# Performance work log

Measured on AMD Instinct MI355X. Metric: run time of the kernel, lower is better.

The kernel has to match this reference:

```python
import jax, jax.numpy as jnp
import numpy as np

B, N, D, H = 1, 4096, 768, 12
HD = D // H
SCALE = HD ** -0.5

def setup_inputs() -> dict:
    key = jax.random.key(0)
    k1, k2, k3 = jax.random.split(key, 3)
    x = jax.random.normal(k1, (B, N, D), dtype=jnp.float32)
    W_qkv = jax.random.normal(k2, (D, 3 * D), dtype=jnp.float32) * (D ** -0.5)
    W_out = jax.random.normal(k3, (D, D), dtype=jnp.float32) * (D ** -0.5)
    b_out = jnp.zeros((D,), dtype=jnp.float32)
    return {"x": x, "W_qkv": W_qkv, "W_out": W_out, "b_out": b_out}

def reference(x, W_qkv, W_out, b_out):
    # qkv projection: (B,N,3D)
    qkv = x @ W_qkv
    q, k, v = jnp.split(qkv, 3, axis=-1)
    # (B,N,D) -> (B,H,N,hd)
    def heads(t):
        return t.reshape(B, N, H, HD).transpose(0, 2, 1, 3)
    q, k, v = heads(q), heads(k), heads(v)
    scores = jnp.einsum('bhnd,bhmd->bhnm', q, k) * SCALE  # (B,H,N,N)
    attn = jax.nn.softmax(scores, axis=-1)
    out = jnp.einsum('bhnm,bhmd->bhnd', attn, v)
    out = out.transpose(0, 2, 1, 3).reshape(B, N, D)
    return out @ W_out + b_out
```

## Files before the change

### kernel.cpp

```cpp
#include <hip/hip_runtime.h>
#include <hip/hip_bf16.h>
#include <math.h>

typedef __attribute__((ext_vector_type(8))) short bf16x8;
typedef __attribute__((ext_vector_type(4))) short bf16x4;
typedef __attribute__((ext_vector_type(4))) float floatx4;

constexpr int kN  = 4096;
constexpr int kD  = 768;
constexpr int kH  = 12;
constexpr int kHD = 64;
constexpr int k3D = 2304;
constexpr float kQScale = 0.18033688011112042f;

static __device__ __forceinline__ short f2b(float f) {
    __hip_bfloat16 h = __float2bfloat16(f);
    return *reinterpret_cast<short*>(&h);
}

static __device__ __forceinline__ float fast_exp2(float x) {
#if __has_builtin(__builtin_amdgcn_exp2f)
    return __builtin_amdgcn_exp2f(x);
#else
    return exp2f(x);
#endif
}

static __device__ __forceinline__ void async_copy16(const void* g, void* l) {
    __builtin_amdgcn_global_load_lds(
        (const __attribute__((address_space(1))) void*)g,
        (__attribute__((address_space(3))) void*)l, 16, 0, 0);
}

constexpr int kBlkX  = 1536;
constexpr int kBlkWq = 72 * 24;
constexpr int kBlkWo = 24 * 24;

__global__ __launch_bounds__(256)
void prep(const float* __restrict__ x, const float* __restrict__ Wq,
          const float* __restrict__ Wo, short* __restrict__ Xb,
          short* __restrict__ WqT, short* __restrict__ WoT)
{
    const int bid = blockIdx.x;
    const int tid = threadIdx.x;
    if (bid < kBlkX) {
        const int i = bid * 256 + tid;
        const float4* s = reinterpret_cast<const float4*>(x + (size_t)i * 8);
        float4 a = s[0], b = s[1];
        bf16x8 v;
        v[0] = f2b(a.x); v[1] = f2b(a.y); v[2] = f2b(a.z); v[3] = f2b(a.w);
        v[4] = f2b(b.x); v[5] = f2b(b.y); v[6] = f2b(b.z); v[7] = f2b(b.w);
        *reinterpret_cast<bf16x8*>(Xb + (size_t)i * 8) = v;
        return;
    }
    const float* src; short* dst; int R, C, bx, by;
    if (bid < kBlkX + kBlkWq) {
        const int local = bid - kBlkX;
        src = Wq; dst = WqT; R = kD; C = k3D; bx = local % 72; by = local / 72;
    } else {
        const int local = bid - kBlkX - kBlkWq;
        src = Wo; dst = WoT; R = kD; C = kD; bx = local % 24; by = local / 24;
    }
    __shared__ float t[32][33];
    const int c0 = bx * 32, r0 = by * 32;
    const int tx = tid & 31, ty = tid >> 5;
    #pragma unroll
    for (int i = ty; i < 32; i += 8)
        t[i][tx] = src[(size_t)(r0 + i) * C + c0 + tx];
    __syncthreads();
    #pragma unroll
    for (int i = ty; i < 32; i += 8)
        dst[(size_t)(c0 + i) * R + r0 + tx] = f2b(t[tx][i]);
}

template<int MODE>
__device__ __forceinline__
void gemm_core(const short* __restrict__ A, const short* __restrict__ BT,
               const float* __restrict__ bias, float* __restrict__ Cout,
               short* __restrict__ Qh, short* __restrict__ Kh, short* __restrict__ Vt,
               int N, int K)
{
    const int bm   = blockIdx.x * 128;
    const int bn   = blockIdx.y * 128;
    const int tid  = threadIdx.x;
    const int wave = tid >> 6;
    const int lane = tid & 63;
    const int l15  = lane & 15;
    const int quad = lane >> 4;
    const int l3   = l15 & 3;

    __shared__ alignas(16) short As[128 * 32];
    __shared__ alignas(16) short Bs[128 * 32];

    floatx4 acc[4][4] = {};
    const int wm = (wave >> 1) * 64;
    const int wn = (wave & 1) * 64;

    const int srl = lane >> 2;
    const int scc = (lane & 3) ^ (srl & 3);

    for (int k0 = 0; k0 < K; k0 += 32) {
        __syncthreads();
        #pragma unroll
        for (int j = 0; j < 2; ++j) {
            const int rs = 32 * wave + 16 * j;
            async_copy16(&A [(size_t)(bm + rs + srl) * K + k0 + 8 * scc], &As[rs * 32]);
            async_copy16(&BT[(size_t)(bn + rs + srl) * K + k0 + 8 * scc], &Bs[rs * 32]);
        }
        __syncthreads();

        bf16x8 af[4], bfr[4];
        #pragma unroll
        for (int mt = 0; mt < 4; ++mt)
            af[mt] = *reinterpret_cast<const bf16x8*>(&As[(wm + 16 * mt + l15) * 32 + 8 * (quad ^ l3)]);
        #pragma unroll
        for (int nt = 0; nt < 4; ++nt)
            bfr[nt] = *reinterpret_cast<const bf16x8*>(&Bs[(wn + 16 * nt + l15) * 32 + 8 * (quad ^ l3)]);
        #pragma unroll
        for (int mt = 0; mt < 4; ++mt)
            #pragma unroll
            for (int nt = 0; nt < 4; ++nt)
                acc[mt][nt] = __builtin_amdgcn_mfma_f32_16x16x32_bf16(af[mt], bfr[nt], acc[mt][nt], 0, 0, 0);
    }

    #pragma unroll
    for (int mt = 0; mt < 4; ++mt) {
        #pragma unroll
        for (int nt = 0; nt < 4; ++nt) {
            #pragma unroll
            for (int r = 0; r < 4; ++r) {
                const int row = bm + wm + mt * 16 + 4 * quad + r;
                const int col = bn + wn + nt * 16 + l15;
                float v = acc[mt][nt][r];
                if (MODE == 0) {
                    Cout[(size_t)row * N + col] = v + bias[col];
                } else {
                    const int proj   = col / kD;
                    const int within = col - proj * kD;
                    const int h = within >> 6;
                    const int d = within & 63;
                    if (proj == 0)      Qh[((size_t)h * kN + row) * kHD + d] = f2b(v * kQScale);
                    else if (proj == 1) Kh[((size_t)h * kN + row) * kHD + d] = f2b(v);
                    else                Vt[((size_t)h * kHD + d) * kN + row] = f2b(v);
                }
            }
        }
    }
}

__global__ __launch_bounds__(256)
void gemm_qkv(const short* __restrict__ A, const short* __restrict__ BT,
              short* __restrict__ Qh, short* __restrict__ Kh, short* __restrict__ Vt)
{
    gemm_core<1>(A, BT, nullptr, nullptr, Qh, Kh, Vt, k3D, kD);
}

__global__ __launch_bounds__(256)
void gemm_out(const short* __restrict__ A, const short* __restrict__ BT,
              const float* __restrict__ bias, float* __restrict__ Cout)
{
    gemm_core<0>(A, BT, bias, Cout, nullptr, nullptr, nullptr, kD, kD);
}

__global__ __launch_bounds__(256, 3)
void attn(const short* __restrict__ Qh, const short* __restrict__ Kh,
          const short* __restrict__ Vt, short* __restrict__ AO)
{
    const int h    = blockIdx.y;
    const int q0   = blockIdx.x * 64;
    const int tid  = threadIdx.x;
    const int wave = tid >> 6;
    const int lane = tid & 63;
    const int l15  = lane & 15;
    const int quad = lane >> 4;
    const int lx   = l15 & 7;
    const int px   = l15 & 3;

    __shared__ alignas(16) char smem[49920];
    short* Ks = (short*)smem;
    short* Vs = (short*)(smem + 16384);
    short* Pm = (short*)(smem + 32768);
    float* Red  = (float*)smem;
    float* Dred = (float*)(smem + 49152);

    short* Pw = Pm + wave * 2048;

    bf16x8 qf[4][2];
    #pragma unroll
    for (int mt = 0; mt < 4; ++mt) {
        const size_t qb = ((size_t)h * kN + q0 + 16 * mt + l15) * kHD + quad * 8;
        qf[mt][0] = *reinterpret_cast<const bf16x8*>(&Qh[qb]);
        qf[mt][1] = *reinterpret_cast<const bf16x8*>(&Qh[qb + 32]);
    }

    floatx4 oacc[4][4] = {};
    float psum[4] = {0.f, 0.f, 0.f, 0.f};

    const int krl = lane >> 3;
    const int kcc = (lane & 7) ^ (krl & 7);
    const int vrl = lane >> 4;
    const int vp  = lane & 15;

    for (int kv0 = 0; kv0 < kN; kv0 += 128) {
        __syncthreads();
        #pragma unroll
        for (int j = 0; j < 4; ++j) {
            const int rk = 32 * wave + 8 * j;
            async_copy16(&Kh[((size_t)h * kN + kv0 + rk + krl) * kHD + 8 * kcc],
                         &Ks[rk * 64]);
            const int rv0 = 16 * wave + 4 * j;
            const int rv  = rv0 + vrl;
            async_copy16(&Vt[((size_t)h * kHD + rv) * kN + kv0 + 8 * (vp ^ (rv & 7))],
                         &Vs[rv0 * 128]);
        }
        __syncthreads();

        #pragma unroll
        for (int nt = 0; nt < 2; ++nt) {
            const int krow = (32 * wave + 16 * nt + l15) * 64;
            bf16x8 kf0 = *reinterpret_cast<const bf16x8*>(&Ks[krow + 8 * (quad ^ lx)]);
            bf16x8 kf1 = *reinterpret_cast<const bf16x8*>(&Ks[krow + 8 * ((4 + quad) ^ lx)]);
            #pragma unroll
            for (int mt = 0; mt < 4; ++mt) {
                floatx4 sa = {};
                sa = __builtin_amdgcn_mfma_f32_16x16x32_bf16(kf0, qf[mt][0], sa, 0, 0, 0);
                sa = __builtin_amdgcn_mfma_f32_16x16x32_bf16(kf1, qf[mt][1], sa, 0, 0, 0);
                const float p0 = fast_exp2(sa[0]);
                const float p1 = fast_exp2(sa[1]);
                const float p2 = fast_exp2(sa[2]);
                const float p3 = fast_exp2(sa[3]);
                psum[mt] += (p0 + p1) + (p2 + p3);
                bf16x4 pk;
                pk[0] = f2b(p0); pk[1] = f2b(p1); pk[2] = f2b(p2); pk[3] = f2b(p3);
                *reinterpret_cast<bf16x4*>(
                    &Pw[(16 * mt + l15) * 32 + 8 * ((2 * nt + (quad >> 1)) ^ px) + 4 * (quad & 1)]) = pk;
            }
        }

        bf16x8 pa[4];
        #pragma unroll
        for (int mt = 0; mt < 4; ++mt)
            pa[mt] = *reinterpret_cast<const bf16x8*>(
                &Pw[(16 * mt + l15) * 32 + 8 * (quad ^ px)]);
        #pragma unroll
        for (int dt = 0; dt < 4; ++dt) {
            bf16x8 vv = *reinterpret_cast<const bf16x8*>(
                &Vs[(16 * dt + l15) * 128 + 8 * ((4 * wave + quad) ^ lx)]);
            #pragma unroll
            for (int mt = 0; mt < 4; ++mt)
                oacc[mt][dt] = __builtin_amdgcn_mfma_f32_16x16x32_bf16(pa[mt], vv, oacc[mt][dt], 0, 0, 0);
        }
    }

    #pragma unroll
    for (int mt = 0; mt < 4; ++mt) {
        psum[mt] += __shfl_xor(psum[mt], 16);
        psum[mt] += __shfl_xor(psum[mt], 32);
    }

    __syncthreads();
    if (wave > 0) {
        float* rb = Red + (wave - 1) * 4096;
        #pragma unroll
        for (int mt = 0; mt < 4; ++mt)
            #pragma unroll
            for (int dt = 0; dt < 4; ++dt)
                *reinterpret_cast<floatx4*>(&rb[((mt * 4 + dt) * 64 + lane) * 4]) = oacc[mt][dt];
        if (lane < 16) {
            #pragma unroll
            for (int mt = 0; mt < 4; ++mt)
                Dred[((wave - 1) * 4 + mt) * 16 + l15] = psum[mt];
        }
    }
    __syncthreads();
    if (wave == 0) {
        #pragma unroll
        for (int w = 0; w < 3; ++w) {
            const float* rb = Red + w * 4096;
            #pragma unroll
            for (int mt = 0; mt < 4; ++mt) {
                #pragma unroll
                for (int dt = 0; dt < 4; ++dt) {
                    floatx4 t = *reinterpret_cast<const floatx4*>(&rb[((mt * 4 + dt) * 64 + lane) * 4]);
                    oacc[mt][dt][0] += t[0];
                    oacc[mt][dt][1] += t[1];
                    oacc[mt][dt][2] += t[2];
                    oacc[mt][dt][3] += t[3];
                }
                psum[mt] += Dred[(w * 4 + mt) * 16 + l15];
            }
        }
        #pragma unroll
        for (int mt = 0; mt < 4; ++mt) {
            float lr[4];
            #pragma unroll
            for (int r = 0; r < 4; ++r)
                lr[r] = __shfl(psum[mt], 4 * quad + r);
            #pragma unroll
            for (int dt = 0; dt < 4; ++dt)
                #pragma unroll
                for (int r = 0; r < 4; ++r)
                    AO[(size_t)(q0 + 16 * mt + 4 * quad + r) * kD + h * kHD + 16 * dt + l15] =
                        f2b(oacc[mt][dt][r] / lr[r]);
        }
    }
}

extern "C" void kernel_launch(void* const* d_in, const int* in_sizes, int n_in,
                              void* d_out, int out_size, void* d_ws, size_t ws_size,
                              hipStream_t stream)
{
    const float* x     = (const float*)d_in[0];
    const float* W_qkv = (const float*)d_in[1];
    const float* W_out = (const float*)d_in[2];
    const float* b_out = (const float*)d_in[3];
    float* out = (float*)d_out;

    const size_t HNHD = (size_t)kH * kN * kHD;
    short* Qh    = (short*)d_ws;
    short* Kh    = Qh + HNHD;
    short* Vt    = Kh + HNHD;
    short* Xb    = Vt + HNHD;
    short* WqkvT = Xb + (size_t)kN * kD;
    short* WoutT = WqkvT + (size_t)k3D * kD;
    short* AO    = Xb;
    (void)in_sizes; (void)n_in; (void)out_size; (void)ws_size;

    prep<<<dim3(kBlkX + kBlkWq + kBlkWo), dim3(256), 0, stream>>>(
        x, W_qkv, W_out, Xb, WqkvT, WoutT);

    gemm_qkv<<<dim3(kN / 128, k3D / 128), dim3(256), 0, stream>>>(
        Xb, WqkvT, Qh, Kh, Vt);
    attn<<<dim3(kN / 64, kH), dim3(256), 0, stream>>>(Qh, Kh, Vt, AO);
    gemm_out<<<dim3(kN / 128, kD / 128), dim3(256), 0, stream>>>(
        AO, WoutT, b_out, out);
}
```

Measured before the change: 202.8 us.

## Load K/V fragments directly from global into registers with K prefetch, drop LDS staging

Attention kernel no longer stages K and V tiles through shared memory with async copies and block barriers. Each wave now reads its K and V MFMA fragments straight from global memory into registers and prefetches the next K tile one iteration ahead. The per-iteration __syncthreads pair is removed. Occupancy hint drops from 3 to 2 blocks per SM to leave room for the extra registers. The cost is scattered, less-coalesced global loads (especially strided V rows), relying on L2/L1 for reuse across the waves.

```diff
diff --git a/kernel.cpp b/kernel.cpp
--- a/kernel.cpp
+++ b/kernel.cpp
@@ -162,7 +162,7 @@
     gemm_core<0>(A, BT, bias, Cout, nullptr, nullptr, nullptr, kD, kD);
 }
 
-__global__ __launch_bounds__(256, 3)
+__global__ __launch_bounds__(256, 2)
 void attn(const short* __restrict__ Qh, const short* __restrict__ Kh,
           const short* __restrict__ Vt, short* __restrict__ AO)
 {
@@ -173,13 +173,10 @@
     const int lane = tid & 63;
     const int l15  = lane & 15;
     const int quad = lane >> 4;
-    const int lx   = l15 & 7;
     const int px   = l15 & 3;
 
     __shared__ alignas(16) char smem[49920];
-    short* Ks = (short*)smem;
-    short* Vs = (short*)(smem + 16384);
-    short* Pm = (short*)(smem + 32768);
+    short* Pm   = (short*)smem;
     float* Red  = (float*)smem;
     float* Dred = (float*)(smem + 49152);
 
@@ -196,35 +193,45 @@
     floatx4 oacc[4][4] = {};
     float psum[4] = {0.f, 0.f, 0.f, 0.f};
 
-    const int krl = lane >> 3;
-    const int kcc = (lane & 7) ^ (krl & 7);
-    const int vrl = lane >> 4;
-    const int vp  = lane & 15;
-
-    for (int kv0 = 0; kv0 < kN; kv0 += 128) {
-        __syncthreads();
-        #pragma unroll
-        for (int j = 0; j < 4; ++j) {
-            const int rk = 32 * wave + 8 * j;
-            async_copy16(&Kh[((size_t)h * kN + kv0 + rk + krl) * kHD + 8 * kcc],
-                         &Ks[rk * 64]);
-            const int rv0 = 16 * wave + 4 * j;
-            const int rv  = rv0 + vrl;
-            async_copy16(&Vt[((size_t)h * kHD + rv) * kN + kv0 + 8 * (vp ^ (rv & 7))],
-                         &Vs[rv0 * 128]);
-        }
-        __syncthreads();
+    const short* kbase_l = Kh + (size_t)h * kN * kHD
+                              + (size_t)(32 * wave + l15) * kHD + 8 * quad;
+    const short* vbase_l = Vt + (size_t)h * kHD * kN
+                              + (size_t)l15 * kN + 32 * wave + 8 * quad;
+
+    bf16x8 kf[4];
+    #pragma unroll
+    for (int nt = 0; nt < 2; ++nt)
+        #pragma unroll
+        for (int s = 0; s < 2; ++s)
+            kf[2 * nt + s] = *reinterpret_cast<const bf16x8*>(
+                kbase_l + (size_t)(16 * nt) * kHD + 32 * s);
+
+    for (int it = 0; it < 32; ++it) {
+        const int kv0 = it * 128;
+
+        bf16x8 vv[4];
+        #pragma unroll
+        for (int dt = 0; dt < 4; ++dt)
+            vv[dt] = *reinterpret_cast<const bf16x8*>(
+                vbase_l + (size_t)(16 * dt) * kN + kv0);
+
+        bf16x8 kn[4];
+        if (it + 1 < 32) {
+            #pragma unroll
+            for (int nt = 0; nt < 2; ++nt)
+                #pragma unroll
+                for (int s = 0; s < 2; ++s)
+                    kn[2 * nt + s] = *reinterpret_cast<const bf16x8*>(
+                        kbase_l + (size_t)(kv0 + 128 + 16 * nt) * kHD + 32 * s);
+        }
 
         #pragma unroll
         for (int nt = 0; nt < 2; ++nt) {
-            const int krow = (32 * wave + 16 * nt + l15) * 64;
-            bf16x8 kf0 = *reinterpret_cast<const bf16x8*>(&Ks[krow + 8 * (quad ^ lx)]);
-            bf16x8 kf1 = *reinterpret_cast<const bf16x8*>(&Ks[krow + 8 * ((4 + quad) ^ lx)]);
             #pragma unroll
             for (int mt = 0; mt < 4; ++mt) {
                 floatx4 sa = {};
-                sa = __builtin_amdgcn_mfma_f32_16x16x32_bf16(kf0, qf[mt][0], sa, 0, 0, 0);
-                sa = __builtin_amdgcn_mfma_f32_16x16x32_bf16(kf1, qf[mt][1], sa, 0, 0, 0);
+                sa = __builtin_amdgcn_mfma_f32_16x16x32_bf16(kf[2 * nt],     qf[mt][0], sa, 0, 0, 0);
+                sa = __builtin_amdgcn_mfma_f32_16x16x32_bf16(kf[2 * nt + 1], qf[mt][1], sa, 0, 0, 0);
                 const float p0 = fast_exp2(sa[0]);
                 const float p1 = fast_exp2(sa[1]);
                 const float p2 = fast_exp2(sa[2]);
@@ -243,13 +250,13 @@
             pa[mt] = *reinterpret_cast<const bf16x8*>(
                 &Pw[(16 * mt + l15) * 32 + 8 * (quad ^ px)]);
         #pragma unroll
-        for (int dt = 0; dt < 4; ++dt) {
-            bf16x8 vv = *reinterpret_cast<const bf16x8*>(
-                &Vs[(16 * dt + l15) * 128 + 8 * ((4 * wave + quad) ^ lx)]);
+        for (int dt = 0; dt < 4; ++dt)
             #pragma unroll
             for (int mt = 0; mt < 4; ++mt)
-                oacc[mt][dt] = __builtin_amdgcn_mfma_f32_16x16x32_bf16(pa[mt], vv, oacc[mt][dt], 0, 0, 0);
-        }
+                oacc[mt][dt] = __builtin_amdgcn_mfma_f32_16x16x32_bf16(pa[mt], vv[dt], oacc[mt][dt], 0, 0, 0);
+
+        #pragma unroll
+        for (int i2 = 0; i2 < 4; ++i2) kf[i2] = kn[i2];
     }
 
     #pragma unroll
```

New measurement: 224.9 us. +10.9%, slower.
